# Kernel tuning notes

Hardware: AMD Instinct MI355X
Metric: run time of the kernel (lower is better)

## Reference

```python
import jax, jax.numpy as jnp
import numpy as np
import math

D_MODEL = 1024
N_HEADS = 16
HEAD_DIM = D_MODEL // N_HEADS


def _compute_slopes(n_heads: int) -> np.ndarray:
    def pow2_slopes(n):
        start = 2.0 ** (-(2.0 ** (-(math.log2(n) - 3))))
        return [start * (start ** i) for i in range(n)]
    if math.log2(n_heads).is_integer():
        s = pow2_slopes(n_heads)
    else:
        cp = 2 ** math.floor(math.log2(n_heads))
        s = pow2_slopes(cp) + pow2_slopes(2 * cp)[0::2][: n_heads - cp]
    return np.asarray(s, dtype=np.float32)


def setup_inputs() -> dict:
    key = jax.random.key(0)
    ks = jax.random.split(key, 11)
    B, T, D = 2, 2048, D_MODEL
    scale = 1.0 / math.sqrt(D)
    inp = {
        "query": jax.random.normal(ks[0], (B, T, D), jnp.float32),
        "key": jax.random.normal(ks[1], (B, T, D), jnp.float32),
        "value": jax.random.normal(ks[2], (B, T, D), jnp.float32),
        "Wq": jax.random.normal(ks[3], (D, D), jnp.float32) * scale,
        "bq": jnp.zeros((D,), jnp.float32),
        "Wk": jax.random.normal(ks[4], (D, D), jnp.float32) * scale,
        "bk": jnp.zeros((D,), jnp.float32),
        "Wv": jax.random.normal(ks[5], (D, D), jnp.float32) * scale,
        "bv": jnp.zeros((D,), jnp.float32),
        "Wo": jax.random.normal(ks[6], (D, D), jnp.float32) * scale,
        "bo": jnp.zeros((D,), jnp.float32),
    }
    return inp


def reference(query, key, value, Wq, bq, Wk, bk, Wv, bv, Wo, bo):
    B, Tq, D = query.shape
    Tk = key.shape[1]
    H, hd = N_HEADS, HEAD_DIM
    scale = hd ** -0.5

    # projections -> [B, H, T, hd]
    Q = (query @ Wq + bq).reshape(B, Tq, H, hd).transpose(0, 2, 1, 3)
    K = (key @ Wk + bk).reshape(B, Tk, H, hd).transpose(0, 2, 1, 3)
    V = (value @ Wv + bv).reshape(B, Tk, H, hd).transpose(0, 2, 1, 3)

    # scores [B, H, Tq, Tk]
    attn = jnp.einsum("bhqd,bhkd->bhqk", Q, K) * scale

    # ALiBi bias (only applied when Tq == Tk, mirroring the original)
    slopes = jnp.asarray(_compute_slopes(H))  # [H]
    pos = jnp.arange(Tq)
    dist = -jnp.abs(pos[None, :] - pos[:, None]).astype(jnp.float32)  # [Tq, Tk]
    bias = slopes[:, None, None] * dist[None]  # [H, Tq, Tk]
    attn = attn + bias[None]

    attn = jax.nn.softmax(attn, axis=-1)
    out = jnp.einsum("bhqk,bhkd->bhqd", attn, V)
    out = out.transpose(0, 2, 1, 3).reshape(B, Tq, D)
    return out @ Wo + bo
```

## Files before the change

### kernel.cpp

```cpp
#include <hip/hip_runtime.h>
#include <stdint.h>

#define BSZ 2
#define TT 2048
#define DD 1024
#define HH 16
#define HD 64

typedef __bf16 bf16x8 __attribute__((ext_vector_type(8)));
typedef float f32x4 __attribute__((ext_vector_type(4)));

#if __has_builtin(__builtin_amdgcn_exp2f)
__device__ __forceinline__ float fexp2(float x) { return __builtin_amdgcn_exp2f(x); }
#else
__device__ __forceinline__ float fexp2(float x) {
    float r; asm("v_exp_f32 %0, %1\n\ts_nop 1" : "=v"(r) : "v"(x)); return r;
}
#endif

__device__ __forceinline__ unsigned short f2bf(float f) {
    union { float f; unsigned u; } c; c.f = f;
    unsigned u = c.u;
    unsigned r = u + 0x7fffu + ((u >> 16) & 1u);
    return (unsigned short)(r >> 16);
}
__device__ __forceinline__ unsigned fasu(float f) {
    union { float f; unsigned u; } c; c.f = f; return c.u;
}

union U4BF { uint4 u; bf16x8 b; };
__device__ __forceinline__ bf16x8 as_bf8(uint4 v) { U4BF c; c.u = v; return c.b; }

#if __has_builtin(__builtin_amdgcn_global_load_lds)
__device__ __forceinline__ void gl_lds16(const ushort* g, ushort* l) {
    __builtin_amdgcn_global_load_lds(
        (const __attribute__((address_space(1))) uint32_t*)g,
        (__attribute__((address_space(3))) uint32_t*)l, 16, 0, 0);
}
#define GLL_LANE 1
#else
__device__ __forceinline__ void gl_lds16_fallback(const ushort* g, ushort* l, int lane) {
    *(uint4*)(l + lane * 8) = *(const uint4*)(g);
}
#define GLL_LANE 0
#endif

__global__ __launch_bounds__(256)
void prep(const float* __restrict__ q, const float* __restrict__ k,
          const float* __restrict__ v,
          const float* __restrict__ W0, const float* __restrict__ W1,
          const float* __restrict__ W2, const float* __restrict__ W3,
          ushort* __restrict__ xq, ushort* __restrict__ xk, ushort* __restrict__ xv,
          ushort* __restrict__ T0, ushort* __restrict__ T1,
          ushort* __restrict__ T2, ushort* __restrict__ T3) {
    __shared__ float sh[32][33];
    const int y = blockIdx.y;
    if (y < 3) {
        const float* in = (y == 0) ? q : (y == 1) ? k : v;
        ushort* out = (y == 0) ? xq : (y == 1) ? xk : xv;
        int i = blockIdx.x * 256 + threadIdx.x;
        float4 val = ((const float4*)in)[i];
        ushort4 o;
        o.x = f2bf(val.x); o.y = f2bf(val.y); o.z = f2bf(val.z); o.w = f2bf(val.w);
        ((ushort4*)out)[i] = o;
    } else {
        const int x = blockIdx.x;
        const float* src; ushort* dst;
        switch (x >> 10) {
            case 0:  src = W0; dst = T0; break;
            case 1:  src = W1; dst = T1; break;
            case 2:  src = W2; dst = T2; break;
            default: src = W3; dst = T3; break;
        }
        const int tile = x & 1023;
        const int k0 = (tile >> 5) * 32, n0 = (tile & 31) * 32;
        const int tx = threadIdx.x & 31, ty = threadIdx.x >> 5;
        #pragma unroll
        for (int p = 0; p < 4; ++p)
            sh[ty + 8 * p][tx] = src[(size_t)(k0 + ty + 8 * p) * DD + n0 + tx];
        __syncthreads();
        #pragma unroll
        for (int p = 0; p < 4; ++p)
            dst[(size_t)(n0 + ty + 8 * p) * DD + k0 + tx] = f2bf(sh[tx][ty + 8 * p]);
    }
}

template<int BM, int OUT_MODE>
__global__ __launch_bounds__(256)
void gemm_mfma(const ushort* __restrict__ A0, const ushort* __restrict__ B0,
               const float* __restrict__ c0, void* __restrict__ d0,
               const ushort* __restrict__ A1, const ushort* __restrict__ B1,
               const float* __restrict__ c1, void* __restrict__ d1,
               const ushort* __restrict__ A2, const ushort* __restrict__ B2,
               const float* __restrict__ c2, void* __restrict__ d2) {
    constexpr int TI = 4;
    constexpr int TJ = (BM == 128) ? 4 : 2;
    constexpr int WC = (BM == 128) ? 2 : 4;
    __shared__ __attribute__((aligned(16))) ushort As[BM][32];
    __shared__ __attribute__((aligned(16))) ushort Bs[128][32];
    const ushort* A; const ushort* Bt; const float* bias; void* outp;
    const int z = blockIdx.z;
    switch (z) {
        case 0:  A = A0; Bt = B0; bias = c0; outp = d0; break;
        case 1:  A = A1; Bt = B1; bias = c1; outp = d1; break;
        default: A = A2; Bt = B2; bias = c2; outp = d2; break;
    }
    const int tid  = threadIdx.x;
    const int lane = tid & 63, w = tid >> 6;
    const int wr = w / WC, wc = w % WC;
    const int ln = lane & 15, quad = lane >> 4;
    const int m0 = blockIdx.y * BM, n0 = blockIdx.x * 128;

    const f32x4 zero = {0.f, 0.f, 0.f, 0.f};
    f32x4 acc[TI][TJ];
    #pragma unroll
    for (int i = 0; i < TI; ++i)
        #pragma unroll
        for (int j = 0; j < TJ; ++j) acc[i][j] = zero;

    const int lr  = lane >> 2;
    const int lc8 = (lane & 3) * 8;

    for (int kb = 0; kb < 1024; kb += 32) {
        #pragma unroll
        for (int it = 0; it < BM / 64; ++it) {
            int r0 = it * 64 + w * 16;
#if GLL_LANE
            gl_lds16(A + (size_t)(m0 + r0 + lr) * 1024 + kb + lc8, &As[r0][0]);
#else
            gl_lds16_fallback(A + (size_t)(m0 + r0 + lr) * 1024 + kb + lc8, &As[r0][0], lane);
#endif
        }
        #pragma unroll
        for (int it = 0; it < 2; ++it) {
            int r0 = it * 64 + w * 16;
#if GLL_LANE
            gl_lds16(Bt + (size_t)(n0 + r0 + lr) * 1024 + kb + lc8, &Bs[r0][0]);
#else
            gl_lds16_fallback(Bt + (size_t)(n0 + r0 + lr) * 1024 + kb + lc8, &Bs[r0][0], lane);
#endif
        }
        __syncthreads();
        bf16x8 af[TI], bfr[TJ];
        #pragma unroll
        for (int i = 0; i < TI; ++i)
            af[i] = as_bf8(*(const uint4*)&As[wr * 64 + i * 16 + ln][quad * 8]);
        #pragma unroll
        for (int j = 0; j < TJ; ++j)
            bfr[j] = as_bf8(*(const uint4*)&Bs[wc * (TJ * 16) + j * 16 + ln][quad * 8]);
        #pragma unroll
        for (int i = 0; i < TI; ++i)
            #pragma unroll
            for (int j = 0; j < TJ; ++j)
                acc[i][j] = __builtin_amdgcn_mfma_f32_16x16x32_bf16(af[i], bfr[j], acc[i][j], 0, 0, 0);
        __syncthreads();
    }

    #pragma unroll
    for (int j = 0; j < TJ; ++j) {
        int n = n0 + wc * (TJ * 16) + j * 16 + ln;
        float bv = bias[n];
        #pragma unroll
        for (int i = 0; i < TI; ++i) {
            int mb = m0 + wr * 64 + i * 16 + quad * 4;
            if (OUT_MODE == 0 && z == 2) {
                int b = mb >> 11, t = mb & 2047, h = n >> 6, d = n & 63;
                ushort4 pk;
                pk.x = f2bf(acc[i][j][0] + bv);
                pk.y = f2bf(acc[i][j][1] + bv);
                pk.z = f2bf(acc[i][j][2] + bv);
                pk.w = f2bf(acc[i][j][3] + bv);
                *(ushort4*)((ushort*)outp + ((size_t)((b * HH + h) * HD + d)) * TT + t) = pk;
            } else {
                #pragma unroll
                for (int r = 0; r < 4; ++r) {
                    int m = mb + r;
                    float v = acc[i][j][r] + bv;
                    if (OUT_MODE == 0) {
                        int b = m >> 11, t = m & 2047, h = n >> 6, d = n & 63;
                        ((ushort*)outp)[(((size_t)(b * HH + h)) * TT + t) * HD + d] = f2bf(v);
                    } else {
                        ((float*)outp)[(size_t)m * 1024 + n] = v;
                    }
                }
            }
        }
    }
}

__global__ __launch_bounds__(256)
void attn_kernel(const ushort* __restrict__ Qh, const ushort* __restrict__ Kh,
                 const ushort* __restrict__ Vtg, ushort* __restrict__ outp) {
    __shared__ __attribute__((aligned(16))) ushort Ks[2][64][64];
    __shared__ __attribute__((aligned(16))) ushort Vs[2][64][64];
    __shared__ __attribute__((aligned(16))) ushort Ps[4][32][72];

    const int tid  = threadIdx.x;
    const int lane = tid & 63, w = tid >> 6;
    const int ln = lane & 15, quad = lane >> 4;
    const int rr = lane >> 3, jj = lane & 7;
    const int sswz = (jj ^ rr) * 8;
    const int l7 = ln & 7;
    const int u0 = (quad ^ l7) * 8;
    const int u1 = u0 ^ 32;

    bf16x8 ones;
    {
        union { ushort us[8]; bf16x8 v; } uu;
        #pragma unroll
        for (int p = 0; p < 8; ++p) uu.us[p] = 0x3F80;
        ones = uu.v;
    }
    const f32x4 zero = {0.f, 0.f, 0.f, 0.f};
    const float c1 = 0.125f * 1.44269504f;

    const int item = blockIdx.x;
    const int h = 15 - (item >> 5);
    const int sub = item & 31;
    const int b = sub & 1;
    const int qt = sub >> 1;
    const int bh = b * 16 + h;
    const int qb0 = qt * 128;
    const int qbw = qb0 + w * 32;
    const float slope2 = exp2f(-0.5f * (float)(h + 1)) * 1.44269504f;
    const size_t base = (size_t)bh * (TT * HD);

    const int D = (int)ceilf(18.0f / slope2);
    int lo = qb0 - D;
    int kt_lo = (lo > 0) ? (lo >> 6) : 0;
    int kt_hi = (qb0 + 128 + D + 63) >> 6;
    if (kt_hi > TT / 64) kt_hi = TT / 64;
    int wl = qbw - D;
    int my_lo = (wl > 0) ? (wl >> 6) : 0;
    if (my_lo < kt_lo) my_lo = kt_lo;
    int my_hi = (qbw + 32 + D + 63) >> 6;
    if (my_hi > kt_hi) my_hi = kt_hi;

    bf16x8 qa[2][2];
    #pragma unroll
    for (int g = 0; g < 2; ++g) {
        const uint4* qp = (const uint4*)(Qh + base + (size_t)(qbw + g * 16 + ln) * HD);
        qa[g][0] = as_bf8(qp[quad]);
        qa[g][1] = as_bf8(qp[4 + quad]);
    }
    f32x4 o[2][4], lsum[2];
    #pragma unroll
    for (int g = 0; g < 2; ++g) {
        lsum[g] = zero;
        #pragma unroll
        for (int dn = 0; dn < 4; ++dn) o[g][dn] = zero;
    }
    float qrf[2][4];
    #pragma unroll
    for (int g = 0; g < 2; ++g)
        #pragma unroll
        for (int r = 0; r < 4; ++r)
            qrf[g][r] = (float)(qbw + g * 16 + quad * 4 + r);

    auto STAGE = [&](int bufi, int kt) {
        #pragma unroll
        for (int ii = 0; ii < 2; ++ii) {
            const int r0 = (w * 2 + ii) * 8;
#if GLL_LANE
            gl_lds16(Kh + base + (size_t)(kt * 64 + r0 + rr) * HD + sswz, &Ks[bufi][r0][0]);
            gl_lds16(Vtg + base + (size_t)(r0 + rr) * TT + kt * 64 + sswz, &Vs[bufi][r0][0]);
#else
            gl_lds16_fallback(Kh + base + (size_t)(kt * 64 + r0 + rr) * HD + sswz, &Ks[bufi][r0][0], lane);
            gl_lds16_fallback(Vtg + base + (size_t)(r0 + rr) * TT + kt * 64 + sswz, &Vs[bufi][r0][0], lane);
#endif
        }
    };

    STAGE(0, kt_lo);
    int buf = 0;
    for (int kt = kt_lo; kt < kt_hi; ++kt) {
        asm volatile("s_waitcnt vmcnt(0)" ::: "memory");
        __syncthreads();
        if (kt + 1 < kt_hi) STAGE(buf ^ 1, kt + 1);

        if (kt >= my_lo && kt < my_hi) {
            f32x4 s[2][4];
            #pragma unroll
            for (int n = 0; n < 4; ++n) {
                bf16x8 b0 = as_bf8(*(const uint4*)&Ks[buf][n * 16 + ln][u0]);
                bf16x8 b1 = as_bf8(*(const uint4*)&Ks[buf][n * 16 + ln][u1]);
                #pragma unroll
                for (int g = 0; g < 2; ++g) {
                    f32x4 zz = zero;
                    zz = __builtin_amdgcn_mfma_f32_16x16x32_bf16(qa[g][0], b0, zz, 0, 0, 0);
                    s[g][n] = __builtin_amdgcn_mfma_f32_16x16x32_bf16(qa[g][1], b1, zz, 0, 0, 0);
                }
            }

            #pragma unroll
            for (int n = 0; n < 4; ++n) {
                float kg = (float)(kt * 64 + n * 16 + ln);
                int bswz = ((2 * n + (ln >> 3)) ^ quad) * 8 + (ln & 7);
                #pragma unroll
                for (int g = 0; g < 2; ++g) {
                    #pragma unroll
                    for (int r = 0; r < 4; ++r) {
                        float d = qrf[g][r] - kg;
                        float arg = fmaf(s[g][n][r], c1, -slope2 * fabsf(d));
                        float p = fexp2(arg);
                        Ps[w][g * 16 + quad * 4 + r][bswz] = (ushort)(fasu(p) >> 16);
                    }
                }
            }

            #pragma unroll
            for (int hf = 0; hf < 2; ++hf) {
                bf16x8 ap0 = as_bf8(*(const uint4*)&Ps[w][ln]     [((hf * 4 + quad) ^ (ln >> 2)) * 8]);
                bf16x8 ap1 = as_bf8(*(const uint4*)&Ps[w][16 + ln][((hf * 4 + quad) ^ (ln >> 2)) * 8]);
                const int uu = hf ? u1 : u0;
                #pragma unroll
                for (int dn = 0; dn < 4; ++dn) {
                    bf16x8 bv = as_bf8(*(const uint4*)&Vs[buf][dn * 16 + ln][uu]);
                    o[0][dn] = __builtin_amdgcn_mfma_f32_16x16x32_bf16(ap0, bv, o[0][dn], 0, 0, 0);
                    o[1][dn] = __builtin_amdgcn_mfma_f32_16x16x32_bf16(ap1, bv, o[1][dn], 0, 0, 0);
                }
                lsum[0] = __builtin_amdgcn_mfma_f32_16x16x32_bf16(ap0, ones, lsum[0], 0, 0, 0);
                lsum[1] = __builtin_amdgcn_mfma_f32_16x16x32_bf16(ap1, ones, lsum[1], 0, 0, 0);
            }
        }
        buf ^= 1;
    }

    #pragma unroll
    for (int g = 0; g < 2; ++g) {
        #pragma unroll
        for (int r = 0; r < 4; ++r) {
            float inv = __builtin_amdgcn_rcpf(lsum[g][r]);
            int q = qbw + g * 16 + quad * 4 + r;
            size_t ob = ((size_t)(b * TT + q)) * DD + h * HD;
            #pragma unroll
            for (int dn = 0; dn < 4; ++dn)
                outp[ob + dn * 16 + ln] = f2bf(o[g][dn][r] * inv);
        }
    }
}

extern "C" void kernel_launch(void* const* d_in, const int* in_sizes, int n_in,
                              void* d_out, int out_size, void* d_ws, size_t ws_size,
                              hipStream_t stream) {
    const float* query = (const float*)d_in[0];
    const float* key   = (const float*)d_in[1];
    const float* value = (const float*)d_in[2];
    const float* Wq = (const float*)d_in[3];
    const float* bq = (const float*)d_in[4];
    const float* Wk = (const float*)d_in[5];
    const float* bk = (const float*)d_in[6];
    const float* Wv = (const float*)d_in[7];
    const float* bv = (const float*)d_in[8];
    const float* Wo = (const float*)d_in[9];
    const float* bo = (const float*)d_in[10];
    float* out = (float*)d_out;

    char* ws = (char*)d_ws;
    const size_t MB = 1024 * 1024;
    ushort* Xq  = (ushort*)(ws + 0);
    ushort* Xk  = (ushort*)(ws + 8 * MB);
    ushort* Xv  = (ushort*)(ws + 16 * MB);
    ushort* Wtq = (ushort*)(ws + 24 * MB);
    ushort* Wtk = (ushort*)(ws + 26 * MB);
    ushort* Wtv = (ushort*)(ws + 28 * MB);
    ushort* Wto = (ushort*)(ws + 30 * MB);
    ushort* Qh  = (ushort*)(ws + 32 * MB);
    ushort* Kh  = (ushort*)(ws + 40 * MB);
    ushort* Vt  = (ushort*)(ws + 48 * MB);
    ushort* attn = (ushort*)(ws + 0);

    prep<<<dim3(4096, 4), 256, 0, stream>>>(query, key, value, Wq, Wk, Wv, Wo,
                                            Xq, Xk, Xv, Wtq, Wtk, Wtv, Wto);

    gemm_mfma<128, 0><<<dim3(8, 32, 3), 256, 0, stream>>>(
        Xq, Wtq, bq, Qh,  Xk, Wtk, bk, Kh,  Xv, Wtv, bv, Vt);

    attn_kernel<<<dim3(512), 256, 0, stream>>>(Qh, Kh, Vt, attn);

    gemm_mfma<64, 1><<<dim3(8, 64, 1), 256, 0, stream>>>(
        attn, Wto, bo, out,  attn, Wto, bo, out,  attn, Wto, bo, out);
}
```

Baseline: 228.8 us.

## Load V fragments directly to registers, drop V LDS staging, reorder blocks

```diff
diff --git a/kernel.cpp b/kernel.cpp
--- a/kernel.cpp
+++ b/kernel.cpp
@@ -192,8 +192,7 @@
 void attn_kernel(const ushort* __restrict__ Qh, const ushort* __restrict__ Kh,
                  const ushort* __restrict__ Vtg, ushort* __restrict__ outp) {
     __shared__ __attribute__((aligned(16))) ushort Ks[2][64][64];
-    __shared__ __attribute__((aligned(16))) ushort Vs[2][64][64];
-    __shared__ __attribute__((aligned(16))) ushort Ps[4][32][72];
+    __shared__ __attribute__((aligned(16))) ushort Ps[4][32][64];
 
     const int tid  = threadIdx.x;
     const int lane = tid & 63, w = tid >> 6;
@@ -214,7 +213,8 @@
     const f32x4 zero = {0.f, 0.f, 0.f, 0.f};
     const float c1 = 0.125f * 1.44269504f;
 
-    const int item = blockIdx.x;
+    const int bid = blockIdx.x;
+    const int item = (bid < 256) ? bid : (767 - bid);
     const int h = 15 - (item >> 5);
     const int sub = item & 31;
     const int b = sub & 1;
@@ -257,16 +257,16 @@
         for (int r = 0; r < 4; ++r)
             qrf[g][r] = (float)(qbw + g * 16 + quad * 4 + r);
 
+    const ushort* vp = Vtg + base + (size_t)ln * TT + quad * 8;
+
     auto STAGE = [&](int bufi, int kt) {
         #pragma unroll
         for (int ii = 0; ii < 2; ++ii) {
             const int r0 = (w * 2 + ii) * 8;
 #if GLL_LANE
             gl_lds16(Kh + base + (size_t)(kt * 64 + r0 + rr) * HD + sswz, &Ks[bufi][r0][0]);
-            gl_lds16(Vtg + base + (size_t)(r0 + rr) * TT + kt * 64 + sswz, &Vs[bufi][r0][0]);
 #else
             gl_lds16_fallback(Kh + base + (size_t)(kt * 64 + r0 + rr) * HD + sswz, &Ks[bufi][r0][0], lane);
-            gl_lds16_fallback(Vtg + base + (size_t)(r0 + rr) * TT + kt * 64 + sswz, &Vs[bufi][r0][0], lane);
 #endif
         }
     };
@@ -279,7 +279,18 @@
         if (kt + 1 < kt_hi) STAGE(buf ^ 1, kt + 1);
 
         if (kt >= my_lo && kt < my_hi) {
+            uint4 vf[8];
+            {
+                const int vo = kt * 64;
+                #pragma unroll
+                for (int dn = 0; dn < 4; ++dn)
+                    #pragma unroll
+                    for (int hf = 0; hf < 2; ++hf)
+                        vf[dn * 2 + hf] = *(const uint4*)(vp + dn * 32768 + vo + hf * 32);
+            }
+
             f32x4 s[2][4];
+            __builtin_amdgcn_s_setprio(1);
             #pragma unroll
             for (int n = 0; n < 4; ++n) {
                 bf16x8 b0 = as_bf8(*(const uint4*)&Ks[buf][n * 16 + ln][u0]);
@@ -291,11 +302,12 @@
                     s[g][n] = __builtin_amdgcn_mfma_f32_16x16x32_bf16(qa[g][1], b1, zz, 0, 0, 0);
                 }
             }
+            __builtin_amdgcn_s_setprio(0);
 
             #pragma unroll
             for (int n = 0; n < 4; ++n) {
                 float kg = (float)(kt * 64 + n * 16 + ln);
-                int bswz = ((2 * n + (ln >> 3)) ^ quad) * 8 + (ln & 7);
+                const int lun = 2 * n + (ln >> 3);
                 #pragma unroll
                 for (int g = 0; g < 2; ++g) {
                     #pragma unroll
@@ -303,25 +315,27 @@
                         float d = qrf[g][r] - kg;
                         float arg = fmaf(s[g][n][r], c1, -slope2 * fabsf(d));
                         float p = fexp2(arg);
+                        const int bswz = ((lun ^ ((quad & 1) * 4 + r)) * 8) + (ln & 7);
                         Ps[w][g * 16 + quad * 4 + r][bswz] = (ushort)(fasu(p) >> 16);
                     }
                 }
             }
 
+            __builtin_amdgcn_s_setprio(1);
             #pragma unroll
             for (int hf = 0; hf < 2; ++hf) {
-                bf16x8 ap0 = as_bf8(*(const uint4*)&Ps[w][ln]     [((hf * 4 + quad) ^ (ln >> 2)) * 8]);
-                bf16x8 ap1 = as_bf8(*(const uint4*)&Ps[w][16 + ln][((hf * 4 + quad) ^ (ln >> 2)) * 8]);
-                const int uu = hf ? u1 : u0;
+                bf16x8 ap0 = as_bf8(*(const uint4*)&Ps[w][ln]     [((hf * 4 + quad) ^ (ln & 7)) * 8]);
+                bf16x8 ap1 = as_bf8(*(const uint4*)&Ps[w][16 + ln][((hf * 4 + quad) ^ (ln & 7)) * 8]);
                 #pragma unroll
                 for (int dn = 0; dn < 4; ++dn) {
-                    bf16x8 bv = as_bf8(*(const uint4*)&Vs[buf][dn * 16 + ln][uu]);
+                    bf16x8 bv = as_bf8(vf[dn * 2 + hf]);
                     o[0][dn] = __builtin_amdgcn_mfma_f32_16x16x32_bf16(ap0, bv, o[0][dn], 0, 0, 0);
                     o[1][dn] = __builtin_amdgcn_mfma_f32_16x16x32_bf16(ap1, bv, o[1][dn], 0, 0, 0);
                 }
                 lsum[0] = __builtin_amdgcn_mfma_f32_16x16x32_bf16(ap0, ones, lsum[0], 0, 0, 0);
                 lsum[1] = __builtin_amdgcn_mfma_f32_16x16x32_bf16(ap1, ones, lsum[1], 0, 0, 0);
             }
+            __builtin_amdgcn_s_setprio(0);
         }
         buf ^= 1;
     }
```

Result: slower. 250.0 us (+9.3%).
